# Kernel optimization log

Hardware: AMD Instinct MI355X
Metric: run time of the kernel (lower is better)

## Reference

```python
import jax, jax.numpy as jnp
import numpy as np

B, S, D, H = 4, 2048, 1024, 16
HD = D // H
SCALE = HD ** -0.5

def setup_inputs() -> dict:
    key = jax.random.key(0)
    k1, k2, k3 = jax.random.split(key, 3)
    x = jax.random.normal(k1, (B, S, D), dtype=jnp.float32)
    W_qkv = jax.random.normal(k2, (D, 3 * D), dtype=jnp.float32) * (D ** -0.5)
    b_qkv = jnp.zeros((3 * D,), dtype=jnp.float32)
    W_proj = jax.random.normal(k3, (D, D), dtype=jnp.float32) * (D ** -0.5)
    b_proj = jnp.zeros((D,), dtype=jnp.float32)
    return {"x": x, "W_qkv": W_qkv, "b_qkv": b_qkv, "W_proj": W_proj, "b_proj": b_proj}

def reference(x, W_qkv, b_qkv, W_proj, b_proj):
    # x: [B,S,D] -> qkv: [B,S,3D] -> [3,B,H,S,hd]
    qkv = x @ W_qkv + b_qkv
    qkv = qkv.reshape(B, S, 3, H, HD).transpose(2, 0, 3, 1, 4)
    q, k, v = qkv[0], qkv[1], qkv[2]
    # naive full attention: [B,H,S,S]
    attn = jnp.einsum('bhqd,bhkd->bhqk', q, k) * SCALE
    attn = jax.nn.softmax(attn, axis=-1)
    out = jnp.einsum('bhqk,bhkd->bhqd', attn, v)
    out = out.transpose(0, 2, 1, 3).reshape(B, S, D)
    return out @ W_proj + b_proj
```

## Files before the change

kernel.cpp:

```cpp
#include <hip/hip_runtime.h>

typedef __bf16 bf16x8 __attribute__((ext_vector_type(8)));
typedef unsigned short ushort8 __attribute__((ext_vector_type(8)));
typedef float floatx4 __attribute__((ext_vector_type(4)));
typedef unsigned int uintx4 __attribute__((ext_vector_type(4)));

__device__ __forceinline__ unsigned short f2bf(float f) {
  unsigned int u = __builtin_bit_cast(unsigned int, f);
  u += 0x7fffu + ((u >> 16) & 1u);
  return (unsigned short)(u >> 16);
}
__device__ __forceinline__ unsigned int pkbf(float a, float b) {
  unsigned int r;
  asm("v_cvt_pk_bf16_f32 %0, %1, %2" : "=v"(r) : "v"(a), "v"(b));
  return r;
}
__device__ __forceinline__ floatx4 MFMA16(bf16x8 a, bf16x8 b, floatx4 c) {
  return __builtin_amdgcn_mfma_f32_16x16x32_bf16(a, b, c, 0, 0, 0);
}

#define GLOAD16(gsrc, ldst)                                                  \
  __builtin_amdgcn_global_load_lds(                                          \
      (const __attribute__((address_space(1))) void*)(gsrc),                 \
      (__attribute__((address_space(3))) void*)(ldst), 16, 0, 0)

__global__ __launch_bounds__(256) void fill_f32(
    float* __restrict__ out, float val, size_t n) {
  const size_t t = (size_t)blockIdx.x * 256 + threadIdx.x;
  for (size_t i = t; i < n; i += (size_t)gridDim.x * 256) out[i] = val;
}

__global__ __launch_bounds__(256) void cvt_f32_bf16(
    const float* __restrict__ in, unsigned short* __restrict__ out) {
  const size_t t = (size_t)blockIdx.x * 256 + threadIdx.x;
  const float4 a = ((const float4*)in)[2 * t];
  const float4 b = ((const float4*)in)[2 * t + 1];
  uintx4 u;
  u[0] = pkbf(a.x, a.y); u[1] = pkbf(a.z, a.w);
  u[2] = pkbf(b.x, b.y); u[3] = pkbf(b.z, b.w);
  *(uintx4*)&out[t * 8] = u;
}

__global__ __launch_bounds__(256) void transpose_w(
    const float* __restrict__ in, unsigned short* __restrict__ out, int C) {
  __shared__ float T[64][65];
  const int tid = threadIdx.x;
  const int r0 = blockIdx.y * 64, c0 = blockIdx.x * 64;
#pragma unroll
  for (int e = 0; e < 4; ++e) {
    const int idx = e * 256 + tid;
    const int row = idx >> 4, cg = idx & 15;
    const float4 f = *(const float4*)&in[(size_t)(r0 + row) * C + c0 + cg * 4];
    T[row][cg * 4] = f.x; T[row][cg * 4 + 1] = f.y;
    T[row][cg * 4 + 2] = f.z; T[row][cg * 4 + 3] = f.w;
  }
  __syncthreads();
#pragma unroll
  for (int e = 0; e < 2; ++e) {
    const int idx = e * 256 + tid;
    const int cc = idx >> 3, rg = idx & 7;
    uintx4 u;
#pragma unroll
    for (int k = 0; k < 4; ++k)
      u[k] = pkbf(T[rg * 8 + 2 * k][cc], T[rg * 8 + 2 * k + 1][cc]);
    *(uintx4*)&out[(size_t)(c0 + cc) * 1024 + r0 + rg * 8] = u;
  }
}

template <int EPI>
__global__ __launch_bounds__(256) void gemm_nt(
    const unsigned short* __restrict__ A, const unsigned short* __restrict__ Bt,
    const float* __restrict__ bias, unsigned short* __restrict__ o0,
    unsigned short* __restrict__ o1, unsigned short* __restrict__ o2,
    float* __restrict__ of, int M, int N, int K) {
  __shared__ __align__(16) unsigned short As[128 * 32];
  __shared__ __align__(16) unsigned short Bs[128 * 32];
  constexpr int NBX = (EPI == 0) ? 24 : 8;
  constexpr int QX = (NBX * 64) / 8;
  const int tid = threadIdx.x;
  const int lane = tid & 63;
  const int w = tid >> 6;
  const int g = lane >> 4, l15 = lane & 15;
  const int wr = w >> 1, wc = w & 1;
  const int orig = blockIdx.y * NBX + blockIdx.x;
  const int wgid = (orig & 7) * QX + (orig >> 3);
  const int m0 = (wgid / NBX) * 128, n0 = (wgid % NBX) * 128;
  const floatx4 fzero = {0.f, 0.f, 0.f, 0.f};
  floatx4 acc[4][4];
#pragma unroll
  for (int i = 0; i < 4; ++i)
#pragma unroll
    for (int j = 0; j < 4; ++j) acc[i][j] = fzero;

  for (int k0 = 0; k0 < K; k0 += 32) {
#pragma unroll
    for (int p = 0; p < 2; ++p) {
      const int j = p * 256 + tid;
      const int row = j >> 2, cg = j & 3;
      const int dstg = p * 256 + (tid & ~63);
      GLOAD16(&A[(size_t)(m0 + row) * K + k0 + cg * 8], &As[dstg * 8]);
      GLOAD16(&Bt[(size_t)(n0 + row) * K + k0 + cg * 8], &Bs[dstg * 8]);
    }
    __syncthreads();
    bf16x8 af[4], bfr[4];
#pragma unroll
    for (int i = 0; i < 4; ++i)
      af[i] = *(const bf16x8*)&As[(wr * 64 + i * 16 + l15) * 32 + g * 8];
#pragma unroll
    for (int j = 0; j < 4; ++j)
      bfr[j] = *(const bf16x8*)&Bs[(wc * 64 + j * 16 + l15) * 32 + g * 8];
#pragma unroll
    for (int i = 0; i < 4; ++i)
#pragma unroll
      for (int j = 0; j < 4; ++j) acc[i][j] = MFMA16(af[i], bfr[j], acc[i][j]);
    __syncthreads();
  }
#pragma unroll
  for (int i = 0; i < 4; ++i) {
#pragma unroll
    for (int j = 0; j < 4; ++j) {
      const int n = n0 + wc * 64 + j * 16 + l15;
      const float bv = bias[n];
      float vv[4];
#pragma unroll
      for (int r = 0; r < 4; ++r) vv[r] = acc[i][j][r] + bv;
      const int mb = m0 + wr * 64 + i * 16 + g * 4;
      if (EPI == 0) {
        const int three = n >> 10, h = (n >> 6) & 15, hd = n & 63;
        const int b = mb >> 11, s = mb & 2047;
        if (three == 2) {
          ushort4 pk;
          pk.x = f2bf(vv[0]); pk.y = f2bf(vv[1]);
          pk.z = f2bf(vv[2]); pk.w = f2bf(vv[3]);
          const int half = (s >> 5) & 1, hi16 = (s >> 4) & 1, gg = (s >> 2) & 3;
          const int col = (s & ~63) + (half * 4 + gg) * 8 + hi16 * 4;
          *(ushort4*)&o2[(((size_t)(b * 16 + h)) * 64 + hd) * 2048 + col] = pk;
        } else {
          const size_t idx0 = (((size_t)(b * 16 + h)) * 2048 + s) * 64 + hd;
#pragma unroll
          for (int r = 0; r < 4; ++r) {
            if (three == 0)
              o0[idx0 + (size_t)r * 64] = f2bf(vv[r] * 0.1803368801f);
            else
              o1[idx0 + (size_t)r * 64] = f2bf(vv[r]);
          }
        }
      } else {
#pragma unroll
        for (int r = 0; r < 4; ++r) of[(size_t)(mb + r) * N + n] = vv[r];
      }
    }
  }
}

__global__ __launch_bounds__(512, 4) void attn_fwd(
    const unsigned short* __restrict__ Q, const unsigned short* __restrict__ Kq,
    const unsigned short* __restrict__ Vt, unsigned short* __restrict__ Ao) {
  __shared__ __align__(16) unsigned short Ks[2][4096];
  __shared__ __align__(16) unsigned short Vs[2][4096];
  const int blk = blockIdx.x;
  const int xcd = blk & 7, idx = blk >> 3;
  const int bh = xcd + 8 * (idx >> 3);
  const int qt = idx & 7;
  const int tid = threadIdx.x;
  const int lane = tid & 63;
  const int w = tid >> 6;
  const int g = lane >> 4, l15 = lane & 15;
  const int q0 = qt * 256 + w * 32;
  const unsigned short* Qp = Q + (size_t)bh * 2048 * 64;
  const unsigned short* Kp = Kq + (size_t)bh * 2048 * 64;
  const unsigned short* Vp = Vt + (size_t)bh * 64 * 2048;

  bf16x8 qf[2][2];
#pragma unroll
  for (int qg = 0; qg < 2; ++qg)
#pragma unroll
    for (int dh = 0; dh < 2; ++dh)
      qf[qg][dh] =
          *(const bf16x8*)&Qp[(size_t)(q0 + qg * 16 + l15) * 64 + dh * 32 + g * 8];

  const floatx4 minit = {-24.f, -24.f, -24.f, -24.f};
  float lpart[2] = {0.0f, 0.0f};
  floatx4 o[2][4];
#pragma unroll
  for (int qg = 0; qg < 2; ++qg)
#pragma unroll
    for (int tl = 0; tl < 4; ++tl) o[qg][tl] = {0.f, 0.f, 0.f, 0.f};

  const int x7 = l15 & 7;
  unsigned koffb[2];
#pragma unroll
  for (int dh = 0; dh < 2; ++dh)
    koffb[dh] = l15 * 128 + (((dh * 4 + g) ^ x7) * 16);
  const char* ksbase = (const char*)&Ks[0][0];
  const char* vsbase = (const char*)&Vs[0][0];

  const int j = tid;
  const int jsrc = (j & ~7) | ((j & 7) ^ ((j >> 3) & 7));
  const unsigned short* ksrc = Kp + jsrc * 8;
  const int vrow = j >> 3, sg = j & 7;
  const unsigned short* vsrc = Vp + (size_t)vrow * 2048 + (size_t)(sg ^ (vrow & 7)) * 8;
  const int dsto = (tid & ~63) * 8;

#define STAGE(BUF, kv0)                                                       \
  do {                                                                        \
    GLOAD16(ksrc + (size_t)(kv0) * 64, &Ks[BUF][dsto]);                       \
    GLOAD16(vsrc + (kv0), &Vs[BUF][dsto]);                                    \
  } while (0)

#define COMPUTE(BUF)                                                          \
  do {                                                                        \
    floatx4 s[2][4];                                                          \
    __builtin_amdgcn_s_setprio(1);                                            \
    _Pragma("unroll") for (int kvf = 0; kvf < 4; ++kvf) {                     \
      bf16x8 kf0 = *(const bf16x8*)(ksbase + (BUF)*8192 + kvf * 2048 +        \
                                    koffb[0]);                                \
      bf16x8 kf1 = *(const bf16x8*)(ksbase + (BUF)*8192 + kvf * 2048 +        \
                                    koffb[1]);                                \
      _Pragma("unroll") for (int qg = 0; qg < 2; ++qg) {                      \
        s[qg][kvf] = MFMA16(kf0, qf[qg][0], minit);                           \
        s[qg][kvf] = MFMA16(kf1, qf[qg][1], s[qg][kvf]);                      \
      }                                                                       \
    }                                                                         \
    __builtin_amdgcn_s_setprio(0);                                            \
    bf16x8 pf[2][2];                                                          \
    _Pragma("unroll") for (int qg = 0; qg < 2; ++qg) {                        \
      float p[4][4];                                                          \
      _Pragma("unroll") for (int kvf = 0; kvf < 4; ++kvf)                     \
          _Pragma("unroll") for (int r = 0; r < 4; ++r) p[kvf][r] =           \
          exp2f(s[qg][kvf][r]);                                               \
      float t8[8];                                                            \
      _Pragma("unroll") for (int e = 0; e < 8; ++e) t8[e] =                   \
          p[e >> 1][(e & 1) * 2] + p[e >> 1][(e & 1) * 2 + 1];                \
      float t4[4];                                                            \
      _Pragma("unroll") for (int e = 0; e < 4; ++e) t4[e] =                   \
          t8[2 * e] + t8[2 * e + 1];                                          \
      lpart[qg] += (t4[0] + t4[1]) + (t4[2] + t4[3]);                         \
      uintx4 wa, wb;                                                          \
      wa[0] = pkbf(p[0][0], p[0][1]); wa[1] = pkbf(p[0][2], p[0][3]);         \
      wa[2] = pkbf(p[1][0], p[1][1]); wa[3] = pkbf(p[1][2], p[1][3]);         \
      wb[0] = pkbf(p[2][0], p[2][1]); wb[1] = pkbf(p[2][2], p[2][3]);         \
      wb[2] = pkbf(p[3][0], p[3][1]); wb[3] = pkbf(p[3][2], p[3][3]);         \
      pf[qg][0] = __builtin_bit_cast(bf16x8, wa);                             \
      pf[qg][1] = __builtin_bit_cast(bf16x8, wb);                             \
    }                                                                         \
    __builtin_amdgcn_s_setprio(1);                                            \
    _Pragma("unroll") for (int tl = 0; tl < 4; ++tl) {                        \
      _Pragma("unroll") for (int C = 0; C < 2; ++C) {                         \
        bf16x8 vf = *(const bf16x8*)(vsbase + (BUF)*8192 + tl * 2048 +        \
                                     koffb[C]);                               \
        o[0][tl] = MFMA16(pf[0][C], vf, o[0][tl]);                            \
        o[1][tl] = MFMA16(pf[1][C], vf, o[1][tl]);                            \
      }                                                                       \
    }                                                                         \
    __builtin_amdgcn_s_setprio(0);                                            \
  } while (0)

  STAGE(0, 0);
  __syncthreads();
#pragma unroll 1
  for (int t0 = 0; t0 < 32; t0 += 2) {
    STAGE(1, (t0 + 1) * 64);
    COMPUTE(0);
    __syncthreads();
    if (t0 + 2 < 32) STAGE(0, (t0 + 2) * 64);
    COMPUTE(1);
    __syncthreads();
  }
#undef STAGE
#undef COMPUTE

  const int b = bh >> 4, h = bh & 15;
#pragma unroll
  for (int qg = 0; qg < 2; ++qg) {
    float l = lpart[qg];
    l += __shfl_xor(l, 16);
    l += __shfl_xor(l, 32);
    const float linv = 1.0f / l;
    float li[4];
#pragma unroll
    for (int r = 0; r < 4; ++r) li[r] = __shfl(linv, (lane & 48) | (g * 4 + r));
#pragma unroll
    for (int tl = 0; tl < 4; ++tl)
#pragma unroll
      for (int r = 0; r < 4; ++r)
        Ao[((size_t)(b * 2048 + q0 + qg * 16 + g * 4 + r)) * 1024 + h * 64 +
           tl * 16 + l15] = f2bf(o[qg][tl][r] * li[r]);
  }
}

extern "C" void kernel_launch(void* const* d_in, const int* in_sizes, int n_in,
                              void* d_out, int out_size, void* d_ws, size_t ws_size,
                              hipStream_t stream) {
  float* outf = (float*)d_out;
  const size_t OUTN = (size_t)8192 * 1024;

  const float *x = nullptr, *Wqkv = nullptr, *bqkv = nullptr, *Wproj = nullptr,
              *bproj = nullptr;
  for (int i = 0; i < n_in; ++i) {
    switch (in_sizes[i]) {
      case 8388608: x = (const float*)d_in[i]; break;
      case 3145728: Wqkv = (const float*)d_in[i]; break;
      case 3072:    bqkv = (const float*)d_in[i]; break;
      case 1048576: Wproj = (const float*)d_in[i]; break;
      case 1024:    bproj = (const float*)d_in[i]; break;
      default: break;
    }
  }
  if (!x || !Wqkv || !bqkv || !Wproj || !bproj || n_in != 5) {
    fill_f32<<<2048, 256, 0, stream>>>(outf, 5000.0f, OUTN);
    return;
  }
  const size_t SZ = (size_t)4 * 16 * 2048 * 64 * 2;
  if (ws_size < 3 * SZ) {
    fill_f32<<<2048, 256, 0, stream>>>(outf, 1000.0f + (float)(ws_size >> 20), OUTN);
    return;
  }

  char* ws = (char*)d_ws;
  unsigned short* xb = (unsigned short*)(ws);
  unsigned short* Kb = (unsigned short*)(ws + SZ);
  unsigned short* Vtb = (unsigned short*)(ws + 2 * SZ);
  unsigned short* Qb = (unsigned short*)d_out;
  unsigned short* Wtq = (unsigned short*)((char*)d_out + SZ);
  unsigned short* Ao = xb;
  unsigned short* Wtp = Kb;

  cvt_f32_bf16<<<4096, 256, 0, stream>>>(x, xb);
  transpose_w<<<dim3(48, 16), 256, 0, stream>>>(Wqkv, Wtq, 3072);
  gemm_nt<0><<<dim3(24, 64), 256, 0, stream>>>(
      xb, Wtq, bqkv, Qb, Kb, Vtb, nullptr, 8192, 3072, 1024);
  attn_fwd<<<512, 512, 0, stream>>>(Qb, Kb, Vtb, Ao);
  transpose_w<<<dim3(16, 16), 256, 0, stream>>>(Wproj, Wtp, 1024);
  gemm_nt<1><<<dim3(8, 64), 256, 0, stream>>>(
      Ao, Wtp, bproj, nullptr, nullptr, nullptr, outf, 8192, 1024, 1024);
}
```

Before: 218.4 us.

## Rewrite GEMMs with 256x128 tiles, triple-buffered LDS pipeline and XOR swizzle

Replaces the single-buffered 128x128, BK=32 GEMM with a 512-thread kernel using 256x128 tiles and BK=64. Global-to-LDS loads are triple-buffered with explicit vmcnt waits, so loads for upcoming stages overlap MFMA compute. An XOR swizzle on the LDS layout avoids bank conflicts, and s_setprio raises priority around the MFMA bursts. The kernel now hardcodes K=1024 and N strides and uses about 147KB of LDS, which limits occupancy to one block per CU.

```diff
diff --git a/kernel.cpp b/kernel.cpp
--- a/kernel.cpp
+++ b/kernel.cpp
@@ -67,54 +67,99 @@
   }
 }
 
-template <int EPI>
-__global__ __launch_bounds__(256) void gemm_nt(
+template <int NBX, int EPI>
+__global__ __launch_bounds__(512) void gemm8p(
     const unsigned short* __restrict__ A, const unsigned short* __restrict__ Bt,
     const float* __restrict__ bias, unsigned short* __restrict__ o0,
     unsigned short* __restrict__ o1, unsigned short* __restrict__ o2,
-    float* __restrict__ of, int M, int N, int K) {
-  __shared__ __align__(16) unsigned short As[128 * 32];
-  __shared__ __align__(16) unsigned short Bs[128 * 32];
-  constexpr int NBX = (EPI == 0) ? 24 : 8;
-  constexpr int QX = (NBX * 64) / 8;
+    float* __restrict__ of) {
+  __shared__ __align__(16) unsigned short As[3][256 * 64];
+  __shared__ __align__(16) unsigned short Bs[3][128 * 64];
   const int tid = threadIdx.x;
   const int lane = tid & 63;
   const int w = tid >> 6;
   const int g = lane >> 4, l15 = lane & 15;
   const int wr = w >> 1, wc = w & 1;
-  const int orig = blockIdx.y * NBX + blockIdx.x;
+  constexpr int QX = 4 * NBX;
+  const int orig = blockIdx.x;
   const int wgid = (orig & 7) * QX + (orig >> 3);
-  const int m0 = (wgid / NBX) * 128, n0 = (wgid % NBX) * 128;
-  const floatx4 fzero = {0.f, 0.f, 0.f, 0.f};
+  const int m0 = (wgid / NBX) * 256, n0 = (wgid % NBX) * 128;
+
   floatx4 acc[4][4];
 #pragma unroll
   for (int i = 0; i < 4; ++i)
 #pragma unroll
-    for (int j = 0; j < 4; ++j) acc[i][j] = fzero;
-
-  for (int k0 = 0; k0 < K; k0 += 32) {
-#pragma unroll
-    for (int p = 0; p < 2; ++p) {
-      const int j = p * 256 + tid;
-      const int row = j >> 2, cg = j & 3;
-      const int dstg = p * 256 + (tid & ~63);
-      GLOAD16(&A[(size_t)(m0 + row) * K + k0 + cg * 8], &As[dstg * 8]);
-      GLOAD16(&Bt[(size_t)(n0 + row) * K + k0 + cg * 8], &Bs[dstg * 8]);
+    for (int j = 0; j < 4; ++j) acc[i][j] = {0.f, 0.f, 0.f, 0.f};
+
+  const unsigned short* asrc[4];
+  const unsigned short* bsrc[2];
+  int adst[4], bdst[2];
+#pragma unroll
+  for (int p = 0; p < 4; ++p) {
+    const int j = p * 512 + tid;
+    const int row = j >> 3, G = j & 7;
+    asrc[p] = A + (size_t)(m0 + row) * 1024 + (size_t)(G ^ (row & 7)) * 8;
+    adst[p] = (j & ~63) * 8;
+  }
+#pragma unroll
+  for (int p = 0; p < 2; ++p) {
+    const int q = p * 512 + tid;
+    const int row = q >> 3, G = q & 7;
+    bsrc[p] = Bt + (size_t)(n0 + row) * 1024 + (size_t)(G ^ (row & 7)) * 8;
+    bdst[p] = (q & ~63) * 8;
+  }
+
+  unsigned aoff[4][2], boff[4][2];
+#pragma unroll
+  for (int i = 0; i < 4; ++i) {
+    const int ra = wr * 64 + i * 16 + l15;
+    const int rb = wc * 64 + i * 16 + l15;
+#pragma unroll
+    for (int kh = 0; kh < 2; ++kh) {
+      aoff[i][kh] = ra * 128 + (((kh * 4 + g) ^ (ra & 7)) * 16);
+      boff[i][kh] = rb * 128 + (((kh * 4 + g) ^ (rb & 7)) * 16);
     }
-    __syncthreads();
-    bf16x8 af[4], bfr[4];
-#pragma unroll
-    for (int i = 0; i < 4; ++i)
-      af[i] = *(const bf16x8*)&As[(wr * 64 + i * 16 + l15) * 32 + g * 8];
-#pragma unroll
-    for (int j = 0; j < 4; ++j)
-      bfr[j] = *(const bf16x8*)&Bs[(wc * 64 + j * 16 + l15) * 32 + g * 8];
-#pragma unroll
-    for (int i = 0; i < 4; ++i)
-#pragma unroll
-      for (int j = 0; j < 4; ++j) acc[i][j] = MFMA16(af[i], bfr[j], acc[i][j]);
-    __syncthreads();
-  }
+  }
+
+  auto STAGE = [&](int buf, int k0) {
+#pragma unroll
+    for (int p = 0; p < 4; ++p) GLOAD16(asrc[p] + k0, &As[buf][adst[p]]);
+#pragma unroll
+    for (int p = 0; p < 2; ++p) GLOAD16(bsrc[p] + k0, &Bs[buf][bdst[p]]);
+  };
+  auto COMPUTE = [&](int buf) {
+    const char* ab = (const char*)As + buf * 32768;
+    const char* bb = (const char*)Bs + buf * 16384;
+#pragma unroll
+    for (int kh = 0; kh < 2; ++kh) {
+      bf16x8 af[4], bfr[4];
+#pragma unroll
+      for (int i = 0; i < 4; ++i) af[i] = *(const bf16x8*)(ab + aoff[i][kh]);
+#pragma unroll
+      for (int j = 0; j < 4; ++j) bfr[j] = *(const bf16x8*)(bb + boff[j][kh]);
+      __builtin_amdgcn_s_setprio(1);
+#pragma unroll
+      for (int i = 0; i < 4; ++i)
+#pragma unroll
+        for (int j = 0; j < 4; ++j) acc[i][j] = MFMA16(af[i], bfr[j], acc[i][j]);
+      __builtin_amdgcn_s_setprio(0);
+    }
+  };
+
+  STAGE(0, 0);
+  STAGE(1, 64);
+#pragma unroll 1
+  for (int t = 0; t < 16; ++t) {
+    if (t < 14)
+      asm volatile("s_waitcnt vmcnt(6)" ::: "memory");
+    else
+      asm volatile("s_waitcnt vmcnt(0)" ::: "memory");
+    __builtin_amdgcn_s_barrier();
+    if (t + 2 < 16) STAGE((t + 2) % 3, (t + 2) * 64);
+    COMPUTE(t % 3);
+    __builtin_amdgcn_s_barrier();
+  }
+
 #pragma unroll
   for (int i = 0; i < 4; ++i) {
 #pragma unroll
@@ -147,7 +192,7 @@
         }
       } else {
 #pragma unroll
-        for (int r = 0; r < 4; ++r) of[(size_t)(mb + r) * N + n] = vv[r];
+        for (int r = 0; r < 4; ++r) of[(size_t)(mb + r) * 1024 + n] = vv[r];
       }
     }
   }
@@ -328,10 +373,10 @@
 
   cvt_f32_bf16<<<4096, 256, 0, stream>>>(x, xb);
   transpose_w<<<dim3(48, 16), 256, 0, stream>>>(Wqkv, Wtq, 3072);
-  gemm_nt<0><<<dim3(24, 64), 256, 0, stream>>>(
-      xb, Wtq, bqkv, Qb, Kb, Vtb, nullptr, 8192, 3072, 1024);
+  gemm8p<24, 0><<<768, 512, 0, stream>>>(
+      xb, Wtq, bqkv, Qb, Kb, Vtb, nullptr);
   attn_fwd<<<512, 512, 0, stream>>>(Qb, Kb, Vtb, Ao);
   transpose_w<<<dim3(16, 16), 256, 0, stream>>>(Wproj, Wtp, 1024);
-  gemm_nt<1><<<dim3(8, 64), 256, 0, stream>>>(
-      Ao, Wtp, bproj, nullptr, nullptr, nullptr, outf, 8192, 1024, 1024);
-}
+  gemm8p<8, 1><<<256, 512, 0, stream>>>(
+      Ao, Wtp, bproj, nullptr, nullptr, nullptr, outf);
+}
```

Result: no change. 215.9 us (-1.1%).
